# Kernel optimization log

Hardware: AMD Instinct MI355X
Metric: run time of the kernel (lower is better)

The kernel has to match this reference:

```python
import jax, jax.numpy as jnp
import numpy as np

N_QUBITS = 10
DIM = 2 ** N_QUBITS
N_POINTS = 64
D_FEAT = 10
N_LAYERS = 5

# bit tables: bits[:, q] = q-th least-significant bit of the state index.
# kron order in the original builds angles[n-1] x ... x angles[0], so angle q acts on bit q.
_bits = ((np.arange(DIM)[:, None] >> np.arange(N_QUBITS)[None, :]) & 1).astype(np.float32)
BITS_C = jnp.asarray(_bits - 0.5)  # (DIM, n): b_q - 1/2 -> rz diag phase coeffs
# crz ring: crz_matrix(i+1,...) is diagonal phase exp(i*theta*b_{i}*(b_{i+1}-1/2)) (control i, target i+1);
# close_ring is control n-1, target 0.
_ctrl = np.concatenate([np.arange(N_QUBITS - 1), [N_QUBITS - 1]])
_tgt = np.concatenate([np.arange(1, N_QUBITS), [0]])
RING_COEF = jnp.asarray(_bits[:, _ctrl] * (_bits[:, _tgt] - 0.5))  # (DIM, n)
H_GATES = jnp.broadcast_to(
    jnp.asarray((np.array([[1, 1], [1, -1]]) / np.sqrt(2)).astype(np.complex64)),
    (N_QUBITS, 2, 2))


def rz_diag(x, start):
    # rz_layer kron order: qubit q gets angle x[(start + n-1-q) % d]; rz = diag(e^{-it/2}, e^{it/2})
    idx = (start + N_QUBITS - 1 - np.arange(N_QUBITS)) % D_FEAT
    return jnp.exp(1j * (BITS_C @ x[idx]))  # (DIM,) complex64


def ring_diag(angles):
    return jnp.exp(1j * (RING_COEF @ angles))  # (DIM,) complex64


def ry_gates(angles):
    c, s = jnp.cos(0.5 * angles), jnp.sin(0.5 * angles)
    # (n, 2, 2): [[c, -s], [s, c]]
    return jnp.stack([jnp.stack([c, -s], -1), jnp.stack([s, c], -1)], -2).astype(jnp.complex64)


def apply_1q(state, gates):
    # apply gates[q] (2x2) to qubit q (axis n-1-q of the (2,)*n reshaped state)
    psi = state.reshape((2,) * N_QUBITS)
    for q in range(N_QUBITS):
        ax = N_QUBITS - 1 - q
        psi = jnp.moveaxis(jnp.tensordot(gates[q], psi, axes=([1], [ax])), 0, ax)
    return psi.reshape(DIM)


def block_f(state, x, bp, start):
    state = apply_1q(state, H_GATES)
    state = state * rz_diag(x, start)
    state = apply_1q(state, ry_gates(bp[0]))
    return state * ring_diag(bp[1])


def adj_block_f(state, x, bp, start):
    state = state * jnp.conj(ring_diag(bp[1]))
    state = apply_1q(state, ry_gates(-bp[0]))  # ry(t)^dagger = ry(-t)
    state = state * jnp.conj(rz_diag(x, start))
    return apply_1q(state, H_GATES)  # H is self-adjoint


def pair_prob(x1, x2, params):
    state = jnp.zeros((DIM,), jnp.complex64).at[0].set(1.0)
    for j in range(N_LAYERS):
        state = block_f(state, x1, params[j], j * N_QUBITS)
    for k in range(N_LAYERS):
        # faithful to original: start = (num_q - k - 1) * num_q (uses num_q, not n_layers)
        state = adj_block_f(state, x2, params[N_LAYERS - 1 - k], (N_QUBITS - k - 1) * N_QUBITS)
    a = state[0]
    return jnp.real(a) ** 2 + jnp.imag(a) ** 2  # |<0|U2^dag U1|0>|^2


def _kta(data, labels, params):
    x1 = jnp.repeat(data, N_POINTS, axis=0)   # point i of each pair
    x2 = jnp.tile(data, (N_POINTS, 1))        # point j of each pair
    k = jax.vmap(pair_prob, in_axes=(0, 0, None))(x1, x2, params)  # (N*N,)
    lm = (labels[:, None] * labels[None, :]).reshape(-1)
    kp = jnp.sum(lm * k)
    return kp / jnp.sqrt(jnp.sum(k * k) * jnp.sum(lm * lm))


def setup_inputs() -> dict:
    key = jax.random.key(0)
    k1, k2, k3 = jax.random.split(key, 3)
    data = jax.random.normal(k1, (N_POINTS, D_FEAT), jnp.float32)
    labels = jnp.where(jax.random.normal(k2, (N_POINTS,)) >= 0, 1.0, -1.0).astype(jnp.float32)
    params = jax.random.uniform(k3, (N_LAYERS, 2, N_QUBITS), jnp.float32, 0.0, 2.0 * np.pi)
    return {"data": data, "labels": labels, "params": params}


def reference(data, labels, params):
    return _kta(data, labels, params)
```

## Files before the change

kernel.cpp:

```cpp
#include <hip/hip_runtime.h>
#include <math.h>

#define NQ 10
#define DIM 1024
#define NPTS 64
#define DFEAT 10
#define NLAYERS 5
#define SREGS 4
#define NPAIR 2080
#define GBLK  (NPAIR / 4)

#define IS2 0.70710678118654752440f

#define PART_OFF ((size_t)NPTS * DIM * sizeof(float2))

__global__ __launch_bounds__(256) void state_kernel(
    const float* __restrict__ data,
    const float* __restrict__ params,
    float2* __restrict__ psi)
{
    const int i    = blockIdx.x;
    const int tid  = threadIdx.x;
    const int lane = tid & 63;
    const int wv   = tid >> 6;

    __shared__ float4 mc[NLAYERS][NQ];
    __shared__ float2 xb[2][16][64];

    if (tid < NLAYERS * NQ) {
        const int L = tid / NQ, q = tid - L * NQ;
        const float xh = 0.5f * data[i * DFEAT + (9 - q)];
        const float cx = __cosf(xh), sx = __sinf(xh);
        float c = 1.f, s = 0.f;
        if (L != NLAYERS - 1) {
            const float th = 0.5f * params[L * 2 * NQ + q];
            c = __cosf(th); s = __sinf(th);
        }
        const float p = (c + s) * IS2, qm = (c - s) * IS2;
        mc[L][q] = make_float4(qm * cx, -p * sx, p * cx, -qm * sx);
    }
    __syncthreads();

    float re[SREGS], im[SREGS];

    {
        float Pr = 1.f, Pi = 0.f;
#pragma unroll 1
        for (int q = 0; q < 8; ++q) {
            const float4 m = mc[0][q];
            const int b = (q < 6) ? ((lane >> q) & 1) : ((wv >> (q - 6)) & 1);
            const float fr = b ? m.z : m.x;
            const float fi = b ? -m.w : m.y;
            const float nr = Pr * fr - Pi * fi;
            const float ni = Pr * fi + Pi * fr;
            Pr = nr; Pi = ni;
        }
        const float4 m8 = mc[0][8], m9 = mc[0][9];
        const float u8r[2] = {m8.x, m8.z}, u8i[2] = {m8.y, -m8.w};
        const float u9r[2] = {m9.x, m9.z}, u9i[2] = {m9.y, -m9.w};
#pragma unroll
        for (int r = 0; r < SREGS; ++r) {
            const int b8 = r & 1, b9 = (r >> 1) & 1;
            const float vr = u8r[b8] * u9r[b9] - u8i[b8] * u9i[b9];
            const float vi = u8r[b8] * u9i[b9] + u8i[b8] * u9r[b9];
            re[r] = Pr * vr - Pi * vi;
            im[r] = Pr * vi + Pi * vr;
        }
    }

    int sp = 0;

#pragma unroll 1
    for (int L = 0; L < NLAYERS; ++L) {
        if (L > 0) {
#pragma unroll 1
            for (int q = 0; q < 6; ++q) {
                const float4 m = mc[L][q];
                const int   b = (lane >> q) & 1;
                const float msr = b ? -m.x : m.x;
                const float msi = m.y;
                const float mpr = m.z;
                const float mpi = b ? -m.w : m.w;
                float pr[SREGS], pi[SREGS];
#pragma unroll
                for (int r = 0; r < SREGS; ++r) {
                    pr[r] = __shfl_xor(re[r], 1 << q, 64);
                    pi[r] = __shfl_xor(im[r], 1 << q, 64);
                }
#pragma unroll
                for (int r = 0; r < SREGS; ++r) {
                    const float nr = msr * re[r] - msi * im[r] + mpr * pr[r] - mpi * pi[r];
                    const float ni = msr * im[r] + msi * re[r] + mpr * pi[r] + mpi * pr[r];
                    re[r] = nr; im[r] = ni;
                }
            }

#pragma unroll 1
            for (int q = 6; q < 8; ++q) {
                const float4 m = mc[L][q];
                const int   b = (wv >> (q - 6)) & 1;
                const float msr = b ? -m.x : m.x;
                const float msi = m.y;
                const float mpr = m.z;
                const float mpi = b ? -m.w : m.w;
#pragma unroll
                for (int r = 0; r < SREGS; ++r)
                    xb[sp][(wv << 2) | r][lane] = make_float2(re[r], im[r]);
                __syncthreads();
                const int pw = wv ^ (1 << (q - 6));
#pragma unroll
                for (int r = 0; r < SREGS; ++r) {
                    const float2 p2 = xb[sp][(pw << 2) | r][lane];
                    const float nr = msr * re[r] - msi * im[r] + mpr * p2.x - mpi * p2.y;
                    const float ni = msr * im[r] + msi * re[r] + mpr * p2.y + mpi * p2.x;
                    re[r] = nr; im[r] = ni;
                }
                sp ^= 1;
            }

#pragma unroll
            for (int q = 8; q < 10; ++q) {
                const int mask = 1 << (q - 8);
                const float4 m = mc[L][q];
                const float m00r = m.x, m00i = m.y, m01r = m.z, m01i = m.w;
                const float m10r = m.z, m10i = -m.w, m11r = -m.x, m11i = m.y;
#pragma unroll
                for (int r = 0; r < SREGS; ++r) {
                    if (!(r & mask)) {
                        const int r1 = r | mask;
                        const float a0r = re[r],  a0i = im[r];
                        const float a1r = re[r1], a1i = im[r1];
                        re[r]  = m00r * a0r - m00i * a0i + m01r * a1r - m01i * a1i;
                        im[r]  = m00r * a0i + m00i * a0r + m01r * a1i + m01i * a1r;
                        re[r1] = m10r * a0r - m10i * a0i + m11r * a1r - m11i * a1i;
                        im[r1] = m10r * a0i + m10i * a0r + m11r * a1i + m11i * a1r;
                    }
                }
            }
        }

        if (L < NLAYERS - 1) {
            const float* rg = params + L * 2 * NQ + NQ;
            float ph[SREGS] = {0.f, 0.f, 0.f, 0.f};
#pragma unroll 1
            for (int n = 0; n < NQ; ++n) {
                const int   nn = (n == 9) ? 0 : (n + 1);
                const float g  = rg[n];
#pragma unroll
                for (int r = 0; r < SREGS; ++r) {
                    const int idx = (r << 8) | (wv << 6) | lane;
                    const float t = (((idx >> nn) & 1) ? 0.5f : -0.5f) * g;
                    ph[r] += ((idx >> n) & 1) ? t : 0.f;
                }
            }
#pragma unroll
            for (int r = 0; r < SREGS; ++r) {
                const float s = __sinf(ph[r]), c = __cosf(ph[r]);
                const float nr = re[r] * c - im[r] * s;
                const float ni = re[r] * s + im[r] * c;
                re[r] = nr; im[r] = ni;
            }
        }
    }

    float2* out = psi + i * DIM;
#pragma unroll
    for (int r = 0; r < SREGS; ++r)
        out[(r << 8) | (wv << 6) | lane] = make_float2(re[r], im[r]);
}

__global__ __launch_bounds__(256) void gram_kernel(
    const float4* __restrict__ psi4,
    const float* __restrict__ labels,
    float* __restrict__ partials)
{
    __shared__ float sm[2][4];
    const int wave = threadIdx.x >> 6;
    const int lane = threadIdx.x & 63;
    const int w    = blockIdx.x * 4 + wave;

    int i = (int)((129.0f - sqrtf(16641.0f - 8.0f * (float)w)) * 0.5f);
    int Ci = 64 * i - ((i * (i - 1)) >> 1);
    while (w < Ci)            { --i; Ci = 64 * i - ((i * (i - 1)) >> 1); }
    while (w >= Ci + 64 - i)  { Ci += 64 - i; ++i; }
    const int j = i + (w - Ci);

    const float4* a = psi4 + i * (DIM / 2);
    const float4* b = psi4 + j * (DIM / 2);

    float zr = 0.f, zi = 0.f;
#pragma unroll
    for (int r = 0; r < 8; ++r) {
        const int k = (r << 6) | lane;
        const float4 av = a[k], bv = b[k];
        zr += bv.x * av.x + bv.y * av.y + bv.z * av.z + bv.w * av.w;
        zi += bv.x * av.y - bv.y * av.x + bv.z * av.w - bv.w * av.z;
    }
#pragma unroll
    for (int off = 32; off; off >>= 1) {
        zr += __shfl_xor(zr, off, 64);
        zi += __shfl_xor(zi, off, 64);
    }

    if (lane == 0) {
        const float k = zr * zr + zi * zi;
        const float wgt = (i == j) ? 1.f : 2.f;
        sm[0][wave] = wgt * labels[i] * labels[j] * k;
        sm[1][wave] = wgt * k * k;
    }
    __syncthreads();
    if (threadIdx.x == 0) {
        partials[2 * blockIdx.x]     = sm[0][0] + sm[0][1] + sm[0][2] + sm[0][3];
        partials[2 * blockIdx.x + 1] = sm[1][0] + sm[1][1] + sm[1][2] + sm[1][3];
    }
}

__global__ __launch_bounds__(256) void reduce_kernel(
    const float* __restrict__ partials,
    const float* __restrict__ labels,
    float* __restrict__ out)
{
    __shared__ float sm[3][4];
    const int tid  = threadIdx.x;
    const int lane = tid & 63;
    const int wave = tid >> 6;

    float slk = 0.f, skk = 0.f, sl2 = 0.f;
    for (int p = tid; p < GBLK; p += 256) {
        slk += partials[2 * p];
        skk += partials[2 * p + 1];
    }
    if (tid < NPTS) { const float l = labels[tid]; sl2 = l * l; }

#pragma unroll
    for (int off = 32; off; off >>= 1) {
        slk += __shfl_xor(slk, off, 64);
        skk += __shfl_xor(skk, off, 64);
        sl2 += __shfl_xor(sl2, off, 64);
    }
    if (lane == 0) { sm[0][wave] = slk; sm[1][wave] = skk; sm[2][wave] = sl2; }
    __syncthreads();
    if (tid == 0) {
        const float a = sm[0][0] + sm[0][1] + sm[0][2] + sm[0][3];
        const float b = sm[1][0] + sm[1][1] + sm[1][2] + sm[1][3];
        const float c = sm[2][0] + sm[2][1] + sm[2][2] + sm[2][3];
        out[0] = a / sqrtf(b * (c * c));
    }
}

extern "C" void kernel_launch(void* const* d_in, const int* in_sizes, int n_in,
                              void* d_out, int out_size, void* d_ws, size_t ws_size,
                              hipStream_t stream) {
    const float* data   = (const float*)d_in[0];
    const float* labels = (const float*)d_in[1];
    const float* params = (const float*)d_in[2];
    float* out = (float*)d_out;

    float2* psi      = (float2*)d_ws;
    float*  partials = (float*)((char*)d_ws + PART_OFF);

    state_kernel <<<NPTS,  256, 0, stream>>>(data, params, psi);
    gram_kernel  <<<GBLK,  256, 0, stream>>>((const float4*)psi, labels, partials);
    reduce_kernel<<<1,     256, 0, stream>>>(partials, labels, out);
}
```

Measured before the change: 76.19 us.

## Fuse state, gram, and reduce kernels into one cooperative kernel

Merges the three kernel launches into a single cooperative kernel of 64 blocks that uses grid.sync between the state-vector build, the pairwise overlap computation, and the final reduction. This removes two launch overheads and the inter-kernel gaps. In exchange, the gram stage runs on only 256 waves that loop over pairs instead of 520 blocks, and two grid-wide barriers are added. It also fully unrolls the six shuffle-based qubit stages through a macro.

```diff
diff --git a/kernel.cpp b/kernel.cpp
--- a/kernel.cpp
+++ b/kernel.cpp
@@ -1,5 +1,8 @@
 #include <hip/hip_runtime.h>
+#include <hip/hip_cooperative_groups.h>
 #include <math.h>
+
+namespace cg = cooperative_groups;
 
 #define NQ 10
 #define DIM 1024
@@ -8,28 +11,55 @@
 #define NLAYERS 5
 #define SREGS 4
 #define NPAIR 2080
-#define GBLK  (NPAIR / 4)
+#define NWAVE 256
 
 #define IS2 0.70710678118654752440f
 
 #define PART_OFF ((size_t)NPTS * DIM * sizeof(float2))
 
-__global__ __launch_bounds__(256) void state_kernel(
+
+#define SHFL_STAGE(Q, M)                                                      \
+    {                                                                         \
+        const int   b   = (lane >> (Q)) & 1;                                  \
+        const float msr = b ? -(M).x : (M).x;                \
+        const float msi = (M).y;                            \
+        const float mpr = (M).z;                            \
+        const float mpi = b ? -(M).w : (M).w;                \
+        float pr[SREGS], pi[SREGS];                                           \
+        _Pragma("unroll")                                                     \
+        for (int r = 0; r < SREGS; ++r) {                                     \
+            pr[r] = __shfl_xor(re[r], 1 << (Q), 64);                          \
+            pi[r] = __shfl_xor(im[r], 1 << (Q), 64);                          \
+        }                                                                     \
+        _Pragma("unroll")                                                     \
+        for (int r = 0; r < SREGS; ++r) {                                     \
+            const float nr = msr * re[r] - msi * im[r] + mpr * pr[r] - mpi * pi[r]; \
+            const float ni = msr * im[r] + msi * re[r] + mpr * pi[r] + mpi * pr[r]; \
+            re[r] = nr; im[r] = ni;                                           \
+        }                                                                     \
+    }
+
+__global__ __launch_bounds__(256) void fused_kernel(
     const float* __restrict__ data,
+    const float* __restrict__ labels,
     const float* __restrict__ params,
-    float2* __restrict__ psi)
+    float2* __restrict__ psi,
+    float* __restrict__ partials,
+    float* __restrict__ out)
 {
-    const int i    = blockIdx.x;
+    cg::grid_group grid = cg::this_grid();
+    const int blk  = blockIdx.x;
     const int tid  = threadIdx.x;
     const int lane = tid & 63;
     const int wv   = tid >> 6;
 
     __shared__ float4 mc[NLAYERS][NQ];
     __shared__ float2 xb[2][16][64];
+    __shared__ float  sm[4][4];
 
     if (tid < NLAYERS * NQ) {
         const int L = tid / NQ, q = tid - L * NQ;
-        const float xh = 0.5f * data[i * DFEAT + (9 - q)];
+        const float xh = 0.5f * data[blk * DFEAT + (9 - q)];
         const float cx = __cosf(xh), sx = __sinf(xh);
         float c = 1.f, s = 0.f;
         if (L != NLAYERS - 1) {
@@ -73,27 +103,10 @@
 #pragma unroll 1
     for (int L = 0; L < NLAYERS; ++L) {
         if (L > 0) {
-#pragma unroll 1
-            for (int q = 0; q < 6; ++q) {
-                const float4 m = mc[L][q];
-                const int   b = (lane >> q) & 1;
-                const float msr = b ? -m.x : m.x;
-                const float msi = m.y;
-                const float mpr = m.z;
-                const float mpi = b ? -m.w : m.w;
-                float pr[SREGS], pi[SREGS];
-#pragma unroll
-                for (int r = 0; r < SREGS; ++r) {
-                    pr[r] = __shfl_xor(re[r], 1 << q, 64);
-                    pi[r] = __shfl_xor(im[r], 1 << q, 64);
-                }
-#pragma unroll
-                for (int r = 0; r < SREGS; ++r) {
-                    const float nr = msr * re[r] - msi * im[r] + mpr * pr[r] - mpi * pi[r];
-                    const float ni = msr * im[r] + msi * re[r] + mpr * pi[r] + mpi * pr[r];
-                    re[r] = nr; im[r] = ni;
-                }
-            }
+            const float4 m0 = mc[L][0], m1 = mc[L][1], m2 = mc[L][2];
+            const float4 m3 = mc[L][3], m4 = mc[L][4], m5 = mc[L][5];
+            SHFL_STAGE(0, m0) SHFL_STAGE(1, m1) SHFL_STAGE(2, m2)
+            SHFL_STAGE(3, m3) SHFL_STAGE(4, m4) SHFL_STAGE(5, m5)
 
 #pragma unroll 1
             for (int q = 6; q < 8; ++q) {
@@ -163,88 +176,74 @@
         }
     }
 
-    float2* out = psi + i * DIM;
-#pragma unroll
-    for (int r = 0; r < SREGS; ++r)
-        out[(r << 8) | (wv << 6) | lane] = make_float2(re[r], im[r]);
-}
-
-__global__ __launch_bounds__(256) void gram_kernel(
-    const float4* __restrict__ psi4,
-    const float* __restrict__ labels,
-    float* __restrict__ partials)
-{
-    __shared__ float sm[2][4];
-    const int wave = threadIdx.x >> 6;
-    const int lane = threadIdx.x & 63;
-    const int w    = blockIdx.x * 4 + wave;
-
-    int i = (int)((129.0f - sqrtf(16641.0f - 8.0f * (float)w)) * 0.5f);
-    int Ci = 64 * i - ((i * (i - 1)) >> 1);
-    while (w < Ci)            { --i; Ci = 64 * i - ((i * (i - 1)) >> 1); }
-    while (w >= Ci + 64 - i)  { Ci += 64 - i; ++i; }
-    const int j = i + (w - Ci);
-
-    const float4* a = psi4 + i * (DIM / 2);
-    const float4* b = psi4 + j * (DIM / 2);
-
-    float zr = 0.f, zi = 0.f;
-#pragma unroll
-    for (int r = 0; r < 8; ++r) {
-        const int k = (r << 6) | lane;
-        const float4 av = a[k], bv = b[k];
-        zr += bv.x * av.x + bv.y * av.y + bv.z * av.z + bv.w * av.w;
-        zi += bv.x * av.y - bv.y * av.x + bv.z * av.w - bv.w * av.z;
-    }
-#pragma unroll
-    for (int off = 32; off; off >>= 1) {
-        zr += __shfl_xor(zr, off, 64);
-        zi += __shfl_xor(zi, off, 64);
-    }
-
-    if (lane == 0) {
-        const float k = zr * zr + zi * zi;
-        const float wgt = (i == j) ? 1.f : 2.f;
-        sm[0][wave] = wgt * labels[i] * labels[j] * k;
-        sm[1][wave] = wgt * k * k;
-    }
-    __syncthreads();
-    if (threadIdx.x == 0) {
-        partials[2 * blockIdx.x]     = sm[0][0] + sm[0][1] + sm[0][2] + sm[0][3];
-        partials[2 * blockIdx.x + 1] = sm[1][0] + sm[1][1] + sm[1][2] + sm[1][3];
-    }
-}
-
-__global__ __launch_bounds__(256) void reduce_kernel(
-    const float* __restrict__ partials,
-    const float* __restrict__ labels,
-    float* __restrict__ out)
-{
-    __shared__ float sm[3][4];
-    const int tid  = threadIdx.x;
-    const int lane = tid & 63;
-    const int wave = tid >> 6;
-
-    float slk = 0.f, skk = 0.f, sl2 = 0.f;
-    for (int p = tid; p < GBLK; p += 256) {
-        slk += partials[2 * p];
-        skk += partials[2 * p + 1];
-    }
-    if (tid < NPTS) { const float l = labels[tid]; sl2 = l * l; }
-
-#pragma unroll
-    for (int off = 32; off; off >>= 1) {
-        slk += __shfl_xor(slk, off, 64);
-        skk += __shfl_xor(skk, off, 64);
-        sl2 += __shfl_xor(sl2, off, 64);
-    }
-    if (lane == 0) { sm[0][wave] = slk; sm[1][wave] = skk; sm[2][wave] = sl2; }
-    __syncthreads();
-    if (tid == 0) {
-        const float a = sm[0][0] + sm[0][1] + sm[0][2] + sm[0][3];
-        const float b = sm[1][0] + sm[1][1] + sm[1][2] + sm[1][3];
-        const float c = sm[2][0] + sm[2][1] + sm[2][2] + sm[2][3];
-        out[0] = a / sqrtf(b * (c * c));
+    {
+        float2* o = psi + blk * DIM;
+#pragma unroll
+        for (int r = 0; r < SREGS; ++r)
+            o[(r << 8) | (wv << 6) | lane] = make_float2(re[r], im[r]);
+    }
+    __threadfence();
+    grid.sync();
+
+    {
+        const float4* psi4 = (const float4*)psi;
+        const int gwave = blk * 4 + wv;
+        float wslk = 0.f, wskk = 0.f;
+
+#pragma unroll 1
+        for (int w = gwave; w < NPAIR; w += NWAVE) {
+            int i = (int)((129.0f - sqrtf(16641.0f - 8.0f * (float)w)) * 0.5f);
+            int Ci = 64 * i - ((i * (i - 1)) >> 1);
+            while (w < Ci)            { --i; Ci = 64 * i - ((i * (i - 1)) >> 1); }
+            while (w >= Ci + 64 - i)  { Ci += 64 - i; ++i; }
+            const int j = i + (w - Ci);
+
+            const float4* a = psi4 + i * (DIM / 2);
+            const float4* b = psi4 + j * (DIM / 2);
+            float zr = 0.f, zi = 0.f;
+#pragma unroll
+            for (int r = 0; r < 8; ++r) {
+                const int k = (r << 6) | lane;
+                const float4 av = a[k], bv = b[k];
+                zr += bv.x * av.x + bv.y * av.y + bv.z * av.z + bv.w * av.w;
+                zi += bv.x * av.y - bv.y * av.x + bv.z * av.w - bv.w * av.z;
+            }
+#pragma unroll
+            for (int off = 32; off; off >>= 1) {
+                zr += __shfl_xor(zr, off, 64);
+                zi += __shfl_xor(zi, off, 64);
+            }
+            const float k   = zr * zr + zi * zi;
+            const float wgt = (i == j) ? 1.f : 2.f;
+            wslk += wgt * labels[i] * labels[j] * k;
+            wskk += wgt * k * k;
+        }
+
+        if (lane == 0) { sm[0][wv] = wslk; sm[1][wv] = wskk; }
+        __syncthreads();
+        if (tid == 0) {
+            partials[2 * blk]     = sm[0][0] + sm[0][1] + sm[0][2] + sm[0][3];
+            partials[2 * blk + 1] = sm[1][0] + sm[1][1] + sm[1][2] + sm[1][3];
+        }
+    }
+    __threadfence();
+    grid.sync();
+
+    if (blk == 0) {
+        float v = 0.f;
+        if (wv == 0)      v = partials[2 * lane];
+        else if (wv == 1) v = partials[2 * lane + 1];
+        else if (wv == 2) { const float l = labels[lane]; v = l * l; }
+#pragma unroll
+        for (int off = 32; off; off >>= 1) v += __shfl_xor(v, off, 64);
+        if (lane == 0) sm[3][wv] = v;
+        __syncthreads();
+        if (tid == 0) {
+            const float slk = sm[3][0];
+            const float skk = sm[3][1];
+            const float sl2 = sm[3][2];
+            out[0] = slk / sqrtf(skk * (sl2 * sl2));
+        }
     }
 }
 
@@ -259,7 +258,8 @@
     float2* psi      = (float2*)d_ws;
     float*  partials = (float*)((char*)d_ws + PART_OFF);
 
-    state_kernel <<<NPTS,  256, 0, stream>>>(data, params, psi);
-    gram_kernel  <<<GBLK,  256, 0, stream>>>((const float4*)psi, labels, partials);
-    reduce_kernel<<<1,     256, 0, stream>>>(partials, labels, out);
+    void* args[] = { (void*)&data, (void*)&labels, (void*)&params,
+                     (void*)&psi, (void*)&partials, (void*)&out };
+    hipLaunchCooperativeKernel((void*)fused_kernel, dim3(NPTS), dim3(256),
+                               args, 0, stream);
 }
```

Result: slower. 118.5 us (+55.6%).
